# Kernel tuning notes

Hardware: AMD Instinct MI355X
Metric: run time of the kernel (lower is better)

Reference implementation:

```python
import jax, jax.numpy as jnp
import numpy as np

N, D = 96, 512
EPS = 1e-8
INV_TEMP = 100.0  # 1 / 0.01


def _pair_indices(n):
    # all ordered pairs (i, j) with i != j, row-major like the original loops
    i, j = np.meshgrid(np.arange(n), np.arange(n), indexing='ij')
    mask = i != j
    return jnp.asarray(i[mask]), jnp.asarray(j[mask])


def setup_inputs() -> dict:
    key = jax.random.key(0)
    k1, k2 = jax.random.split(key)
    return {
        "txtf": jax.random.normal(k1, (N, D), dtype=jnp.float32),
        "imgf": jax.random.normal(k2, (N, D), dtype=jnp.float32),
    }


def reference(txtf, imgf):
    n = txtf.shape[0]
    ii, jj = _pair_indices(n)  # [P], P = n*(n-1)

    td = txtf[ii] - txtf[jj]                                   # [P, D]
    td = td / (jnp.linalg.norm(td, axis=-1, keepdims=True) + EPS)
    im = imgf[ii] - imgf[jj]                                   # [P, D]
    im = im / (jnp.linalg.norm(im, axis=-1, keepdims=True) + EPS)

    mma = jnp.einsum('pd,qd->pq', td, im) * INV_TEMP           # [P, P]
    diag = jnp.arange(mma.shape[0])
    # CE(mma, labels): softmax over rows; CE(mma.T, labels): softmax over cols
    lp_row = jax.nn.log_softmax(mma, axis=-1)
    lp_col = jax.nn.log_softmax(mma, axis=0)
    loss1 = -jnp.mean(lp_row[diag, diag])
    loss2 = -jnp.mean(lp_col[diag, diag])
    return (loss1 + loss2) * 0.5
```

## Files before the change

### kernel.cpp

```cpp
#include <hip/hip_runtime.h>
#include <math.h>

#define NN 96
#define DD 512
#define PP 9120
#define EPSF 1e-8f
#define INV_TEMP 100.0f
#define LOG2E 1.4426950408889634f
#define RT 8
#define NTASK (2*PP)
#define NBLK (NTASK/RT)
#define CBASE (PP/RT)

typedef float v2f __attribute__((ext_vector_type(2)));

#define OFF_PART  0
#define OFF_G     55296
#define OFF_GT    64512
#define OFF_WT    73728
#define OFF_WM    82944
#define OFF_WST   92160
#define OFF_WSM   101376
#define OFF_DIAG  110592
#define OFF_WMAX  119712
#define OFF_BSUM  119720

__device__ __forceinline__ void decomp(unsigned p, int& i, int& j) {
    unsigned ii = p / 95u;
    unsigned r  = p - ii * 95u;
    i = (int)ii;
    j = (int)(r + (r >= ii ? 1u : 0u));
}

__global__ __launch_bounds__(256) void gram_kernel(const float* __restrict__ txt,
                                                   const float* __restrict__ img,
                                                   float* __restrict__ ws) {
    __shared__ float4 Al[16][65];
    __shared__ float4 Bl[16][65];
    int zz = blockIdx.z;
    int z = zz >> 1, ks = zz & 1;
    int a0 = blockIdx.x * 16, b0 = blockIdx.y * 16;
    const float* X = (z == 2) ? img : txt;
    const float* Y = (z == 0) ? img : ((z == 1) ? txt : img);
    const float4* Xp = (const float4*)X;
    const float4* Yp = (const float4*)Y;
    int tid = threadIdx.x;
    int r = tid >> 6, c = tid & 63;
    int kbase = ks * 64;
    #pragma unroll
    for (int rep = 0; rep < 4; ++rep) {
        int row = rep * 4 + r;
        Al[row][c] = Xp[(a0 + row) * 128 + kbase + c];
        Bl[row][c] = Yp[(b0 + row) * 128 + kbase + c];
    }
    __syncthreads();
    int al = tid >> 4, bl = tid & 15;
    float acc = 0.f;
    #pragma unroll 8
    for (int kk = 0; kk < 64; ++kk) {
        float4 av = Al[al][kk];
        float4 bv = Bl[bl][kk];
        acc += av.x*bv.x + av.y*bv.y + av.z*bv.z + av.w*bv.w;
    }
    ws[OFF_PART + zz * (NN*NN) + (a0 + al) * NN + (b0 + bl)] = acc;
}

__global__ void pairs_kernel(float* __restrict__ ws) {
    int t = blockIdx.x * 256 + threadIdx.x;
    int k = t / NN, l = t - k * NN;
    const float* P = ws + OFF_PART;
    #define RD(z, x) (P[(2*(z)) * (NN*NN) + (x)] + P[(2*(z)+1) * (NN*NN) + (x)])
    float gkl = RD(0, k*NN + l);
    float glk = RD(0, l*NN + k);
    ws[OFF_G  + t] = gkl;
    ws[OFF_GT + t] = glk;
    float wtv = 0.f, wmv = 0.f;
    if (k != l) {
        float nt2 = RD(1, k*NN+k) - 2.f*RD(1, k*NN+l) + RD(1, l*NN+l);
        float nm2 = RD(2, k*NN+k) - 2.f*RD(2, k*NN+l) + RD(2, l*NN+l);
        wtv = 1.f / (sqrtf(fmaxf(nt2, 0.f)) + EPSF);
        wmv = 1.f / (sqrtf(fmaxf(nm2, 0.f)) + EPSF);
        int p = k * 95 + l - (l > k ? 1 : 0);
        float gkk = RD(0, k*NN+k), gll = RD(0, l*NN+l);
        ws[OFF_DIAG + p] = INV_TEMP * wtv * wmv * (gkk - gkl - glk + gll);
    }
    #undef RD
    ws[OFF_WT  + t] = wtv;
    ws[OFF_WM  + t] = wmv;
    ws[OFF_WST + t] = wtv * LOG2E;
    ws[OFF_WSM + t] = wmv * LOG2E;
    float mt = wtv, mm = wmv;
    #pragma unroll
    for (int off = 32; off > 0; off >>= 1) {
        mt = fmaxf(mt, __shfl_xor(mt, off, 64));
        mm = fmaxf(mm, __shfl_xor(mm, off, 64));
    }
    if ((threadIdx.x & 63) == 0) {
        atomicMax((unsigned int*)(ws + OFF_WMAX) + 0, __float_as_uint(mt));
        atomicMax((unsigned int*)(ws + OFF_WMAX) + 1, __float_as_uint(mm));
    }
}

__global__ __launch_bounds__(256) void lse_kernel(float* __restrict__ ws) {
    __shared__ float A[RT * NN];
    __shared__ float M2s[RT];
    __shared__ float Ms[RT];
    __shared__ float wred[4][RT];
    __shared__ float cred[RT];

    int tid = threadIdx.x, lane = tid & 63, wv = tid >> 6;
    int b = blockIdx.x;
    bool is_col = (b >= CBASE);
    const float* Mat    = ws + (is_col ? OFF_GT  : OFF_G);
    const float* wself  = ws + (is_col ? OFF_WM  : OFF_WT);
    const float* wsweep = ws + (is_col ? OFF_WST : OFF_WSM);
    float Wmax = __uint_as_float(((const unsigned int*)(ws + OFF_WMAX))[is_col ? 0 : 1]);
    int base = (b - (is_col ? CBASE : 0)) * RT;

    #pragma unroll
    for (int q = 0; q < 2; ++q) {
        int rr = 2 * wv + q;
        int i, j; decomp((unsigned)(base + rr), i, j);
        float s = INV_TEMP * wself[i * NN + j];
        const float* Mi = Mat + i * NN;
        const float* Mj = Mat + j * NN;
        float v0 = s * (Mi[lane] - Mj[lane]);
        A[rr * NN + lane] = v0;
        float vmax = v0, vmin = v0;
        if (lane < 32) {
            float v1 = s * (Mi[64 + lane] - Mj[64 + lane]);
            A[rr * NN + 64 + lane] = v1;
            vmax = fmaxf(vmax, v1); vmin = fminf(vmin, v1);
        }
        #pragma unroll
        for (int off = 32; off > 0; off >>= 1) {
            vmax = fmaxf(vmax, __shfl_xor(vmax, off, 64));
            vmin = fminf(vmin, __shfl_xor(vmin, off, 64));
        }
        if (lane == 0) {
            float M = Wmax * (vmax - vmin);
            Ms[rr] = M;
            M2s[rr] = M * LOG2E;
        }
    }
    __syncthreads();

    int l1 = (lane < 32) ? (64 + lane) : (lane - 32);
    float M2[RT], aL1r[RT], S1[RT];
    v2f aL02[RT], S2[RT];
    #pragma unroll
    for (int r = 0; r < RT; ++r) {
        M2[r] = M2s[r];
        aL02[r].x = A[r * NN + lane];
        aL02[r].y = A[r * NN + lane + 32];
        aL1r[r] = A[r * NN + l1];
        S1[r] = 0.f;
        S2[r] = (v2f){0.f, 0.f};
    }

    for (int idx = wv; idx < 48; idx += 4) {
        int k0 = 2 * idx, k1 = k0 + 1;
        v2f w02;
        w02.x = wsweep[k0 * NN + lane];
        float w1 = wsweep[(lane < 32 ? k0 : k1) * NN + l1];
        w02.y = wsweep[k1 * NN + lane + 32];
        #pragma unroll
        for (int r = 0; r < RT; ++r) {
            v2f ak = *(const v2f*)&A[r * NN + k0];
            float aksel = (lane < 32) ? ak.x : ak.y;
            v2f arg = w02 * (ak - aL02[r]);
            arg.x -= M2[r]; arg.y -= M2[r];
            v2f e;
            e.x = __builtin_amdgcn_exp2f(arg.x);
            e.y = __builtin_amdgcn_exp2f(arg.y);
            S2[r] += e;
            S1[r] += __builtin_amdgcn_exp2f(w1 * (aksel - aL1r[r]) - M2[r]);
        }
    }

    float S[RT];
    #pragma unroll
    for (int r = 0; r < RT; ++r) S[r] = S1[r] + S2[r].x + S2[r].y;
    #pragma unroll
    for (int off = 32; off > 0; off >>= 1) {
        #pragma unroll
        for (int r = 0; r < RT; ++r) S[r] += __shfl_xor(S[r], off, 64);
    }
    if (lane == 0) {
        #pragma unroll
        for (int r = 0; r < RT; ++r) wred[wv][r] = S[r];
    }
    __syncthreads();

    if (tid < RT) {
        int r = tid;
        float tot = wred[0][r] + wred[1][r] + wred[2][r] + wred[3][r];
        tot -= 96.f * __builtin_amdgcn_exp2f(-M2s[r]);
        cred[r] = Ms[r] + logf(tot) - ws[OFF_DIAG + base + r];
    }
    __syncthreads();
    if (tid == 0) {
        float c = 0.f;
        #pragma unroll
        for (int r = 0; r < RT; ++r) c += cred[r];
        ws[OFF_BSUM + b] = c;
    }
}

__global__ void final_kernel(const float* __restrict__ ws, float* __restrict__ out) {
    __shared__ float red[256];
    int tid = threadIdx.x;
    float s = 0.f;
    for (int i = tid; i < NBLK; i += 256)
        s += ws[OFF_BSUM + i];
    red[tid] = s; __syncthreads();
    for (int t = 128; t > 0; t >>= 1) {
        if (tid < t) red[tid] += red[tid + t];
        __syncthreads();
    }
    if (tid == 0) out[0] = red[0] * (1.0f / (float)NTASK);
}

extern "C" void kernel_launch(void* const* d_in, const int* in_sizes, int n_in,
                              void* d_out, int out_size, void* d_ws, size_t ws_size,
                              hipStream_t stream) {
    const float* txt = (const float*)d_in[0];
    const float* img = (const float*)d_in[1];
    float* ws = (float*)d_ws;

    (void)hipMemsetAsync(ws + OFF_WMAX, 0, 2 * sizeof(float), stream);
    gram_kernel<<<dim3(6, 6, 6), 256, 0, stream>>>(txt, img, ws);
    pairs_kernel<<<36, 256, 0, stream>>>(ws);
    lse_kernel<<<NBLK, 256, 0, stream>>>(ws);
    final_kernel<<<1, 256, 0, stream>>>(ws, (float*)d_out);
}
```

Before: 99.93 us.

## Exploit antisymmetry of pair rows and fuse final reduction via atomics

Row (j,i) of the logit matrix is the negation of row (i,j), so each block now processes only unordered pairs (k<l) and accumulates exp sums for both the positive and negated arguments, halving the A-row construction and weight loads per task. A lookup table of unordered pairs built in pairs_kernel replaces the division-based index decomposition. The separate memset and final reduction kernel are removed: gram_kernel zeroes the max slots and output, and lse blocks atomically add into the output. This changes float summation order and adds atomic contention on a single address.

After: 100.8 us. Within noise of the previous version (+0.9%).

```diff
diff --git a/kernel.cpp b/kernel.cpp
--- a/kernel.cpp
+++ b/kernel.cpp
@@ -4,13 +4,14 @@
 #define NN 96
 #define DD 512
 #define PP 9120
+#define NUP 4560
 #define EPSF 1e-8f
 #define INV_TEMP 100.0f
 #define LOG2E 1.4426950408889634f
-#define RT 8
+#define RP 4
 #define NTASK (2*PP)
-#define NBLK (NTASK/RT)
-#define CBASE (PP/RT)
+#define NBLK (2*NUP/RP)
+#define CBASE (NUP/RP)
 
 typedef float v2f __attribute__((ext_vector_type(2)));
 
@@ -23,20 +24,19 @@
 #define OFF_WSM   101376
 #define OFF_DIAG  110592
 #define OFF_WMAX  119712
-#define OFF_BSUM  119720
-
-__device__ __forceinline__ void decomp(unsigned p, int& i, int& j) {
-    unsigned ii = p / 95u;
-    unsigned r  = p - ii * 95u;
-    i = (int)ii;
-    j = (int)(r + (r >= ii ? 1u : 0u));
-}
+#define OFF_TAB   119714
 
 __global__ __launch_bounds__(256) void gram_kernel(const float* __restrict__ txt,
                                                    const float* __restrict__ img,
-                                                   float* __restrict__ ws) {
+                                                   float* __restrict__ ws,
+                                                   float* __restrict__ out) {
     __shared__ float4 Al[16][65];
     __shared__ float4 Bl[16][65];
+    if (blockIdx.x == 0 && blockIdx.y == 0 && blockIdx.z == 0 && threadIdx.x == 0) {
+        ws[OFF_WMAX] = 0.f;
+        ws[OFF_WMAX + 1] = 0.f;
+        out[0] = 0.f;
+    }
     int zz = blockIdx.z;
     int z = zz >> 1, ks = zz & 1;
     int a0 = blockIdx.x * 16, b0 = blockIdx.y * 16;
@@ -83,6 +83,10 @@
         int p = k * 95 + l - (l > k ? 1 : 0);
         float gkk = RD(0, k*NN+k), gll = RD(0, l*NN+l);
         ws[OFF_DIAG + p] = INV_TEMP * wtv * wmv * (gkk - gkl - glk + gll);
+        if (k < l) {
+            int q = k * (2*NN - 1 - k) / 2 + (l - k - 1);
+            ((int*)ws)[OFF_TAB + q] = (k << 8) | l;
+        }
     }
     #undef RD
     ws[OFF_WT  + t] = wtv;
@@ -101,12 +105,13 @@
     }
 }
 
-__global__ __launch_bounds__(256) void lse_kernel(float* __restrict__ ws) {
-    __shared__ float A[RT * NN];
-    __shared__ float M2s[RT];
-    __shared__ float Ms[RT];
-    __shared__ float wred[4][RT];
-    __shared__ float cred[RT];
+__global__ __launch_bounds__(256) void lse_kernel(float* __restrict__ ws,
+                                                  float* __restrict__ out) {
+    __shared__ float A[RP * NN];
+    __shared__ float M2s[RP];
+    __shared__ float Ms[RP];
+    __shared__ float wred[4][2 * RP];
+    __shared__ float cred[2 * RP];
 
     int tid = threadIdx.x, lane = tid & 63, wv = tid >> 6;
     int b = blockIdx.x;
@@ -115,21 +120,21 @@
     const float* wself  = ws + (is_col ? OFF_WM  : OFF_WT);
     const float* wsweep = ws + (is_col ? OFF_WST : OFF_WSM);
     float Wmax = __uint_as_float(((const unsigned int*)(ws + OFF_WMAX))[is_col ? 0 : 1]);
-    int base = (b - (is_col ? CBASE : 0)) * RT;
-
-    #pragma unroll
-    for (int q = 0; q < 2; ++q) {
-        int rr = 2 * wv + q;
-        int i, j; decomp((unsigned)(base + rr), i, j);
+    int qbase = (b - (is_col ? CBASE : 0)) * RP;
+    const int* tab = (const int*)ws + OFF_TAB;
+
+    {
+        int pk = tab[qbase + wv];
+        int i = pk >> 8, j = pk & 255;
         float s = INV_TEMP * wself[i * NN + j];
         const float* Mi = Mat + i * NN;
         const float* Mj = Mat + j * NN;
         float v0 = s * (Mi[lane] - Mj[lane]);
-        A[rr * NN + lane] = v0;
+        A[wv * NN + lane] = v0;
         float vmax = v0, vmin = v0;
         if (lane < 32) {
             float v1 = s * (Mi[64 + lane] - Mj[64 + lane]);
-            A[rr * NN + 64 + lane] = v1;
+            A[wv * NN + 64 + lane] = v1;
             vmax = fmaxf(vmax, v1); vmin = fminf(vmin, v1);
         }
         #pragma unroll
@@ -139,23 +144,24 @@
         }
         if (lane == 0) {
             float M = Wmax * (vmax - vmin);
-            Ms[rr] = M;
-            M2s[rr] = M * LOG2E;
+            Ms[wv] = M;
+            M2s[wv] = M * LOG2E;
         }
     }
     __syncthreads();
 
     int l1 = (lane < 32) ? (64 + lane) : (lane - 32);
-    float M2[RT], aL1r[RT], S1[RT];
-    v2f aL02[RT], S2[RT];
-    #pragma unroll
-    for (int r = 0; r < RT; ++r) {
+    float M2[RP], aL1r[RP], S1p[RP], S1m[RP];
+    v2f aL02[RP], S2p[RP], S2m[RP];
+    #pragma unroll
+    for (int r = 0; r < RP; ++r) {
         M2[r] = M2s[r];
         aL02[r].x = A[r * NN + lane];
         aL02[r].y = A[r * NN + lane + 32];
         aL1r[r] = A[r * NN + l1];
-        S1[r] = 0.f;
-        S2[r] = (v2f){0.f, 0.f};
+        S1p[r] = 0.f; S1m[r] = 0.f;
+        S2p[r] = (v2f){0.f, 0.f};
+        S2m[r] = (v2f){0.f, 0.f};
     }
 
     for (int idx = wv; idx < 48; idx += 4) {
@@ -165,60 +171,56 @@
         float w1 = wsweep[(lane < 32 ? k0 : k1) * NN + l1];
         w02.y = wsweep[k1 * NN + lane + 32];
         #pragma unroll
-        for (int r = 0; r < RT; ++r) {
+        for (int r = 0; r < RP; ++r) {
             v2f ak = *(const v2f*)&A[r * NN + k0];
             float aksel = (lane < 32) ? ak.x : ak.y;
-            v2f arg = w02 * (ak - aL02[r]);
-            arg.x -= M2[r]; arg.y -= M2[r];
-            v2f e;
-            e.x = __builtin_amdgcn_exp2f(arg.x);
-            e.y = __builtin_amdgcn_exp2f(arg.y);
-            S2[r] += e;
-            S1[r] += __builtin_amdgcn_exp2f(w1 * (aksel - aL1r[r]) - M2[r]);
-        }
-    }
-
-    float S[RT];
-    #pragma unroll
-    for (int r = 0; r < RT; ++r) S[r] = S1[r] + S2[r].x + S2[r].y;
+            v2f t02 = w02 * (ak - aL02[r]);
+            v2f e, f;
+            e.x = __builtin_amdgcn_exp2f(t02.x - M2[r]);
+            e.y = __builtin_amdgcn_exp2f(t02.y - M2[r]);
+            f.x = __builtin_amdgcn_exp2f(-t02.x - M2[r]);
+            f.y = __builtin_amdgcn_exp2f(-t02.y - M2[r]);
+            S2p[r] += e;
+            S2m[r] += f;
+            float t1 = w1 * (aksel - aL1r[r]);
+            S1p[r] += __builtin_amdgcn_exp2f(t1 - M2[r]);
+            S1m[r] += __builtin_amdgcn_exp2f(-t1 - M2[r]);
+        }
+    }
+
+    float S[2 * RP];
+    #pragma unroll
+    for (int r = 0; r < RP; ++r) {
+        S[r]      = S1p[r] + S2p[r].x + S2p[r].y;
+        S[RP + r] = S1m[r] + S2m[r].x + S2m[r].y;
+    }
     #pragma unroll
     for (int off = 32; off > 0; off >>= 1) {
         #pragma unroll
-        for (int r = 0; r < RT; ++r) S[r] += __shfl_xor(S[r], off, 64);
+        for (int r = 0; r < 2 * RP; ++r) S[r] += __shfl_xor(S[r], off, 64);
     }
     if (lane == 0) {
         #pragma unroll
-        for (int r = 0; r < RT; ++r) wred[wv][r] = S[r];
-    }
-    __syncthreads();
-
-    if (tid < RT) {
-        int r = tid;
-        float tot = wred[0][r] + wred[1][r] + wred[2][r] + wred[3][r];
+        for (int r = 0; r < 2 * RP; ++r) wred[wv][r] = S[r];
+    }
+    __syncthreads();
+
+    if (tid < 2 * RP) {
+        int r = tid & (RP - 1);
+        float tot = wred[0][tid] + wred[1][tid] + wred[2][tid] + wred[3][tid];
         tot -= 96.f * __builtin_amdgcn_exp2f(-M2s[r]);
-        cred[r] = Ms[r] + logf(tot) - ws[OFF_DIAG + base + r];
+        int pk = tab[qbase + r];
+        int i = pk >> 8, j = pk & 255;
+        int p = i * 95 + j - 1;
+        cred[tid] = Ms[r] + logf(tot) - ws[OFF_DIAG + p];
     }
     __syncthreads();
     if (tid == 0) {
         float c = 0.f;
         #pragma unroll
-        for (int r = 0; r < RT; ++r) c += cred[r];
-        ws[OFF_BSUM + b] = c;
-    }
-}
-
-__global__ void final_kernel(const float* __restrict__ ws, float* __restrict__ out) {
-    __shared__ float red[256];
-    int tid = threadIdx.x;
-    float s = 0.f;
-    for (int i = tid; i < NBLK; i += 256)
-        s += ws[OFF_BSUM + i];
-    red[tid] = s; __syncthreads();
-    for (int t = 128; t > 0; t >>= 1) {
-        if (tid < t) red[tid] += red[tid + t];
-        __syncthreads();
-    }
-    if (tid == 0) out[0] = red[0] * (1.0f / (float)NTASK);
+        for (int r = 0; r < 2 * RP; ++r) c += cred[r];
+        atomicAdd(out, c * (1.0f / (float)NTASK));
+    }
 }
 
 extern "C" void kernel_launch(void* const* d_in, const int* in_sizes, int n_in,
@@ -227,10 +229,9 @@
     const float* txt = (const float*)d_in[0];
     const float* img = (const float*)d_in[1];
     float* ws = (float*)d_ws;
-
-    (void)hipMemsetAsync(ws + OFF_WMAX, 0, 2 * sizeof(float), stream);
-    gram_kernel<<<dim3(6, 6, 6), 256, 0, stream>>>(txt, img, ws);
+    float* out = (float*)d_out;
+
+    gram_kernel<<<dim3(6, 6, 6), 256, 0, stream>>>(txt, img, ws, out);
     pairs_kernel<<<36, 256, 0, stream>>>(ws);
-    lse_kernel<<<NBLK, 256, 0, stream>>>(ws);
-    final_kernel<<<1, 256, 0, stream>>>(ws, (float*)d_out);
-}
+    lse_kernel<<<NBLK, 256, 0, stream>>>(ws, out);
+}
```
